# Performance work log

Measured on AMD Instinct MI355X. Metric: run time of the kernel, lower is better.

## Reference

```python
import jax, jax.numpy as jnp
import numpy as np

NEG_SLOPE = 0.1
K = 3  # kernel_size

def lrelu(x):
    return jnp.where(x >= 0, x, NEG_SLOPE * x)

def setup_inputs() -> dict:
    key = jax.random.key(0)
    ks = jax.random.split(key, 10)
    B, C, H, W = 16, 64, 128, 128
    DEG, RED = 512, 8
    s = 0.02
    return {
        "feat": jax.random.normal(ks[0], (B, C, H, W), jnp.float32),
        "deg": jax.random.normal(ks[1], (B, DEG, 8, 8), jnp.float32),
        # adaptive_size: Linear(deg_fsize -> C), no bias; torch weight [out,in]
        "W_size": jax.random.normal(ks[2], (C, DEG), jnp.float32) * s,
        # kernel net: Linear(C -> C//red), Linear(C//red -> C*K*K)
        "W_k1": jax.random.normal(ks[3], (C // RED, C), jnp.float32) * s,
        "W_k2": jax.random.normal(ks[4], (C * K * K, C // RED), jnp.float32) * s,
        # 1x1 conv C_in -> C_out with bias (stored as [out,in])
        "W_conv": jax.random.normal(ks[5], (C, C), jnp.float32) * s,
        "b_conv": jax.random.normal(ks[6], (C,), jnp.float32) * s,
        # CA layer: 1x1 conv deg_fsize -> C, then C -> C//red -> C
        "W_ac": jax.random.normal(ks[7], (C, DEG), jnp.float32) * s,
        "W_du1": jax.random.normal(ks[8], (C // RED, C), jnp.float32) * s,
        "W_du2": jax.random.normal(ks[9], (C, C // RED), jnp.float32) * s,
    }

def reference(feat, deg, W_size, W_k1, W_k2, W_conv, b_conv, W_ac, W_du1, W_du2):
    b, c, h, w = feat.shape
    # degradation pooled to a vector: AdaptiveAvgPool2d((1,1)) == mean over HW
    dvec = deg.mean(axis=(2, 3))                      # [B, deg_fsize]
    f = dvec @ W_size.T                               # [B, C]
    # per-sample dynamic depthwise kernels
    kern = lrelu(f @ W_k1.T) @ W_k2.T                 # [B, C*K*K]
    kern = kern.reshape(b * c, 1, K, K)               # [B*C, 1, K, K]
    out = jax.lax.conv_general_dilated(
        feat.reshape(1, b * c, h, w), kern,
        window_strides=(1, 1), padding=[((K - 1) // 2,) * 2] * 2,
        feature_group_count=b * c,
        dimension_numbers=("NCHW", "OIHW", "NCHW"))
    out = lrelu(out).reshape(b, c, h, w)
    # trailing 1x1 conv with bias
    out = jnp.einsum("bchw,oc->bohw", out, W_conv) + b_conv[None, :, None, None]
    # CA branch
    fa = dvec @ W_ac.T                                # [B, C]
    att = jax.nn.sigmoid(lrelu(fa @ W_du1.T) @ W_du2.T)  # [B, C_out]
    return out + feat * att[:, :, None, None]
```

## Files before the change

### kernel.cpp

```cpp
#include <hip/hip_runtime.h>
#include <math.h>

#define NEG_SLOPE 0.1f

typedef __attribute__((ext_vector_type(8))) short short8;
typedef __attribute__((ext_vector_type(4))) short short4v;
typedef __attribute__((ext_vector_type(4))) float floatx4;

__device__ __forceinline__ float lrelu(float x) { return x >= 0.0f ? x : NEG_SLOPE * x; }

__device__ __forceinline__ unsigned short f2bf(float x) {
  unsigned u = __float_as_uint(x);
  return (unsigned short)((u + 0x7fffu + ((u >> 16) & 1u)) >> 16);
}

__device__ __forceinline__ float wave_sum64(float v) {
  #pragma unroll
  for (int s = 32; s > 0; s >>= 1) v += __shfl_xor(v, s, 64);
  return v;
}

__global__ __launch_bounds__(256) void prep1_kernel(
    const float* __restrict__ deg, float* __restrict__ dvec_ws) {
  const int k = blockIdx.x;
  const int b = k >> 2, quar = k & 3;
  const int t = threadIdx.x;
  const int rw = t >> 1, half = t & 1;
  const int d = quar * 128 + rw;
  const float* p = deg + (size_t)b * 32768 + (size_t)d * 64 + half * 32;
  float4 x0 = *(const float4*)(p);
  float4 x1 = *(const float4*)(p + 4);
  float4 x2 = *(const float4*)(p + 8);
  float4 x3 = *(const float4*)(p + 12);
  float4 x4 = *(const float4*)(p + 16);
  float4 x5 = *(const float4*)(p + 20);
  float4 x6 = *(const float4*)(p + 24);
  float4 x7 = *(const float4*)(p + 28);
  float s = (x0.x + x0.y + x0.z + x0.w) + (x1.x + x1.y + x1.z + x1.w) +
            (x2.x + x2.y + x2.z + x2.w) + (x3.x + x3.y + x3.z + x3.w) +
            (x4.x + x4.y + x4.z + x4.w) + (x5.x + x5.y + x5.z + x5.w) +
            (x6.x + x6.y + x6.z + x6.w) + (x7.x + x7.y + x7.z + x7.w);
  s += __shfl_xor(s, 1, 64);
  if (half == 0) dvec_ws[b * 512 + d] = s * (1.0f / 64.0f);
}

__global__ __launch_bounds__(256) void prep2_kernel(
    const float* __restrict__ dvec_ws, const float* __restrict__ W_size,
    const float* __restrict__ W_ac, float* __restrict__ f_ws,
    float* __restrict__ fa_ws) {
  const int k = blockIdx.x;
  const int b = k >> 2, cq = k & 3;
  const int t = threadIdx.x;
  const int cl = t >> 4, sub = t & 15;
  const int c = cq * 16 + cl;
  const float* dv = dvec_ws + b * 512;
  const float* w1 = W_size + (size_t)c * 512;
  const float* w2 = W_ac + (size_t)c * 512;
  float p1 = 0.0f, p2 = 0.0f;
  #pragma unroll
  for (int kk = 0; kk < 8; ++kk) {
    const int e = sub * 4 + kk * 64;
    float4 d  = *(const float4*)(dv + e);
    float4 a  = *(const float4*)(w1 + e);
    float4 bq = *(const float4*)(w2 + e);
    p1 += d.x * a.x + d.y * a.y + d.z * a.z + d.w * a.w;
    p2 += d.x * bq.x + d.y * bq.y + d.z * bq.z + d.w * bq.w;
  }
  #pragma unroll
  for (int s = 1; s < 16; s <<= 1) {
    p1 += __shfl_xor(p1, s, 64);
    p2 += __shfl_xor(p2, s, 64);
  }
  if (sub == 0) { f_ws[b * 64 + c] = p1; fa_ws[b * 64 + c] = p2; }
}

__global__ __launch_bounds__(256) void prep3_kernel(
    const float* __restrict__ f_ws, const float* __restrict__ fa_ws,
    const float* __restrict__ W_k1, const float* __restrict__ W_k2,
    const float* __restrict__ W_du1, const float* __restrict__ W_du2,
    float* __restrict__ kern_ws, float* __restrict__ att_ws) {
  const int b = blockIdx.x;
  const int t = threadIdx.x;
  __shared__ float t1s[8], t2s[8];
  const int wave = t >> 6, lane = t & 63;
  if (wave == 0) {
    float v = f_ws[b * 64 + lane];
    #pragma unroll
    for (int rr = 0; rr < 8; ++rr) {
      float p = wave_sum64(v * W_k1[rr * 64 + lane]);
      if (lane == 0) t1s[rr] = lrelu(p);
    }
  } else if (wave == 1) {
    float v = fa_ws[b * 64 + lane];
    #pragma unroll
    for (int rr = 0; rr < 8; ++rr) {
      float p = wave_sum64(v * W_du1[rr * 64 + lane]);
      if (lane == 0) t2s[rr] = lrelu(p);
    }
  }
  __syncthreads();
  for (int i = t; i < 576; i += 256) {
    float4 wa0 = *(const float4*)&W_k2[i * 8];
    float4 wa1 = *(const float4*)&W_k2[i * 8 + 4];
    kern_ws[b * 576 + i] =
        t1s[0] * wa0.x + t1s[1] * wa0.y + t1s[2] * wa0.z + t1s[3] * wa0.w +
        t1s[4] * wa1.x + t1s[5] * wa1.y + t1s[6] * wa1.z + t1s[7] * wa1.w;
  }
  if (t < 64) {
    float4 wa0 = *(const float4*)&W_du2[t * 8];
    float4 wa1 = *(const float4*)&W_du2[t * 8 + 4];
    float s = t2s[0] * wa0.x + t2s[1] * wa0.y + t2s[2] * wa0.z + t2s[3] * wa0.w +
              t2s[4] * wa1.x + t2s[5] * wa1.y + t2s[6] * wa1.z + t2s[7] * wa1.w;
    att_ws[b * 64 + t] = 1.0f / (1.0f + expf(-s));
  }
}

__global__ __launch_bounds__(256, 4) void fused_kernel(
    const float* __restrict__ feat, const float* __restrict__ W_conv,
    const float* __restrict__ b_conv, const float* __restrict__ kern_ws,
    const float* __restrict__ att_ws, float* __restrict__ out) {
  const int bid = blockIdx.x;
  const int xcd = bid & 7;
  const int idx = bid >> 3;
  const int b = idx >> 3;
  const int sub = idx & 7;
  const int h_base = xcd * 16 + sub * 2;

  const int t = threadIdx.x;

  __shared__ __align__(16) unsigned short zT[128 * 72];
  __shared__ __align__(16) unsigned short wt[64 * 72];
  __shared__ float ks[576];
  __shared__ float atts[64];
  __shared__ float bcs[64];

  {
    const int o = t >> 2;
    const int c0 = (t & 3) * 16;
    const float* wp = W_conv + o * 64 + c0;
    float4 a0 = *(const float4*)(wp);
    float4 a1 = *(const float4*)(wp + 4);
    float4 a2 = *(const float4*)(wp + 8);
    float4 a3 = *(const float4*)(wp + 12);
    const int sw = ((o >> 2) ^ (o >> 5)) & 7;
    short8 p0, p1;
    p0[0] = f2bf(a0.x); p0[1] = f2bf(a0.y); p0[2] = f2bf(a0.z); p0[3] = f2bf(a0.w);
    p0[4] = f2bf(a1.x); p0[5] = f2bf(a1.y); p0[6] = f2bf(a1.z); p0[7] = f2bf(a1.w);
    p1[0] = f2bf(a2.x); p1[1] = f2bf(a2.y); p1[2] = f2bf(a2.z); p1[3] = f2bf(a2.w);
    p1[4] = f2bf(a3.x); p1[5] = f2bf(a3.y); p1[6] = f2bf(a3.z); p1[7] = f2bf(a3.w);
    const int kc0 = ((c0 >> 3) + 0) ^ sw;
    const int kc1 = ((c0 >> 3) + 1) ^ sw;
    *(short8*)&wt[o * 72 + kc0 * 8] = p0;
    *(short8*)&wt[o * 72 + kc1 * 8] = p1;
  }
  for (int i = t; i < 576; i += 256) ks[i] = kern_ws[b * 576 + i];
  if (t < 64) { atts[t] = att_ws[b * 64 + t]; bcs[t] = b_conv[t]; }
  __syncthreads();

  const size_t base_b = (size_t)b * 64 * 128 * 128;
  const int lane = t & 63, wave = t >> 6;
  const int cq = t >> 5;
  const int gg = t & 31;
  const int w0 = gg * 4;
  const int swz = (gg ^ (gg >> 3)) & 7;
  const float4 zf4 = {0.f, 0.f, 0.f, 0.f};

  #pragma unroll 1
  for (int ti = 0; ti < 2; ++ti) {
    const int h = h_base + ti;
    const bool hgt0 = (h > 0), hlt = (h < 127);
    const float* fbase = feat + base_b + (size_t)h * 128 + w0;

    #pragma unroll
    for (int it = 0; it < 2; ++it) {
      const int c0 = cq * 4 + it * 32;
      float4 top[4], mid[4], bot[4];
      #pragma unroll
      for (int j = 0; j < 4; ++j) {
        const float* p = fbase + (size_t)(c0 + j) * 16384;
        mid[j] = *(const float4*)p;
        top[j] = hgt0 ? *(const float4*)(p - 128) : zf4;
        bot[j] = hlt  ? *(const float4*)(p + 128) : zf4;
      }
      unsigned short sres[4][4];
      #pragma unroll
      for (int j = 0; j < 4; ++j) {
        const float* kv = &ks[(c0 + j) * 9];
        const float k0 = kv[0], k1 = kv[1], k2 = kv[2];
        const float k3 = kv[3], k4 = kv[4], k5 = kv[5];
        const float k6 = kv[6], k7 = kv[7], k8 = kv[8];
        float a0 = 0.f, a1 = 0.f, a2 = 0.f, a3 = 0.f;
        {
          float4 m = top[j];
          float lf = __shfl(m.w, lane - 1, 64); if (gg == 0)  lf = 0.f;
          float rt = __shfl(m.x, lane + 1, 64); if (gg == 31) rt = 0.f;
          a0 += k0 * lf  + k1 * m.x + k2 * m.y;
          a1 += k0 * m.x + k1 * m.y + k2 * m.z;
          a2 += k0 * m.y + k1 * m.z + k2 * m.w;
          a3 += k0 * m.z + k1 * m.w + k2 * rt;
        }
        {
          float4 m = mid[j];
          float lf = __shfl(m.w, lane - 1, 64); if (gg == 0)  lf = 0.f;
          float rt = __shfl(m.x, lane + 1, 64); if (gg == 31) rt = 0.f;
          a0 += k3 * lf  + k4 * m.x + k5 * m.y;
          a1 += k3 * m.x + k4 * m.y + k5 * m.z;
          a2 += k3 * m.y + k4 * m.z + k5 * m.w;
          a3 += k3 * m.z + k4 * m.w + k5 * rt;
        }
        {
          float4 m = bot[j];
          float lf = __shfl(m.w, lane - 1, 64); if (gg == 0)  lf = 0.f;
          float rt = __shfl(m.x, lane + 1, 64); if (gg == 31) rt = 0.f;
          a0 += k6 * lf  + k7 * m.x + k8 * m.y;
          a1 += k6 * m.x + k7 * m.y + k8 * m.z;
          a2 += k6 * m.y + k7 * m.z + k8 * m.w;
          a3 += k6 * m.z + k7 * m.w + k8 * rt;
        }
        sres[j][0] = f2bf(lrelu(a0));
        sres[j][1] = f2bf(lrelu(a1));
        sres[j][2] = f2bf(lrelu(a2));
        sres[j][3] = f2bf(lrelu(a3));
      }
      const int chunk = (cq >> 1) + it * 4;
      const int kcs = ((chunk ^ swz) * 8) + (cq & 1) * 4;
      #pragma unroll
      for (int i = 0; i < 4; ++i) {
        short4v sv;
        sv[0] = (short)sres[0][i]; sv[1] = (short)sres[1][i];
        sv[2] = (short)sres[2][i]; sv[3] = (short)sres[3][i];
        *(short4v*)&zT[(w0 + i) * 72 + kcs] = sv;
      }
    }
    __syncthreads();

    {
      const int r = lane & 15, q = lane >> 4;

      short8 az[2][2];
      #pragma unroll
      for (int wm2 = 0; wm2 < 2; ++wm2) {
        const int w = (wave * 2 + wm2) * 16 + r;
        const int sz = ((w >> 2) ^ (w >> 5)) & 7;
        #pragma unroll
        for (int ksp = 0; ksp < 2; ++ksp) {
          const int kc = (ksp * 4 + q) ^ sz;
          az[wm2][ksp] = *(const short8*)&zT[w * 72 + kc * 8];
        }
      }
      short8 bw[4][2];
      #pragma unroll
      for (int nt = 0; nt < 4; ++nt) {
        const int o = nt * 16 + r;
        const int so = ((o >> 2) ^ (o >> 5)) & 7;
        #pragma unroll
        for (int ksp = 0; ksp < 2; ++ksp) {
          const int kc = (ksp * 4 + q) ^ so;
          bw[nt][ksp] = *(const short8*)&wt[o * 72 + kc * 8];
        }
      }

      floatx4 acc[2][4];
      #pragma unroll
      for (int wm2 = 0; wm2 < 2; ++wm2)
        #pragma unroll
        for (int nt = 0; nt < 4; ++nt) acc[wm2][nt] = (floatx4){0.f, 0.f, 0.f, 0.f};

      #pragma unroll
      for (int wm2 = 0; wm2 < 2; ++wm2)
        #pragma unroll
        for (int nt = 0; nt < 4; ++nt)
          #pragma unroll
          for (int ksp = 0; ksp < 2; ++ksp)
            acc[wm2][nt] = __builtin_amdgcn_mfma_f32_16x16x32_bf16(
                az[wm2][ksp], bw[nt][ksp], acc[wm2][nt], 0, 0, 0);

      #pragma unroll
      for (int wm2 = 0; wm2 < 2; ++wm2) {
        const int wb = (wave * 2 + wm2) * 16 + q * 4;
        #pragma unroll
        for (int nt = 0; nt < 4; ++nt) {
          const int o = nt * 16 + r;
          const size_t off = base_b + (size_t)o * 16384 + (size_t)h * 128 + wb;
          float4 fv = *(const float4*)(feat + off);
          const float at = atts[o], bo = bcs[o];
          floatx4 a = acc[wm2][nt];
          float4 ov;
          ov.x = a[0] + bo + at * fv.x;
          ov.y = a[1] + bo + at * fv.y;
          ov.z = a[2] + bo + at * fv.z;
          ov.w = a[3] + bo + at * fv.w;
          *(float4*)(out + off) = ov;
        }
      }
    }
    if (ti == 0) __syncthreads();
  }
}

extern "C" void kernel_launch(void* const* d_in, const int* in_sizes, int n_in,
                              void* d_out, int out_size, void* d_ws, size_t ws_size,
                              hipStream_t stream) {
  const float* feat   = (const float*)d_in[0];
  const float* deg    = (const float*)d_in[1];
  const float* W_size = (const float*)d_in[2];
  const float* W_k1   = (const float*)d_in[3];
  const float* W_k2   = (const float*)d_in[4];
  const float* W_conv = (const float*)d_in[5];
  const float* b_conv = (const float*)d_in[6];
  const float* W_ac   = (const float*)d_in[7];
  const float* W_du1  = (const float*)d_in[8];
  const float* W_du2  = (const float*)d_in[9];
  float* out = (float*)d_out;

  float* dvec_ws = (float*)d_ws;
  float* f_ws    = dvec_ws + 16 * 512;
  float* fa_ws   = f_ws + 16 * 64;
  float* kern_ws = fa_ws + 16 * 64;
  float* att_ws  = kern_ws + 16 * 576;

  prep1_kernel<<<64, 256, 0, stream>>>(deg, dvec_ws);
  prep2_kernel<<<64, 256, 0, stream>>>(dvec_ws, W_size, W_ac, f_ws, fa_ws);
  prep3_kernel<<<16, 256, 0, stream>>>(f_ws, fa_ws, W_k1, W_k2, W_du1, W_du2,
                                       kern_ws, att_ws);
  fused_kernel<<<1024, 256, 0, stream>>>(feat, W_conv, b_conv, kern_ws, att_ws,
                                         out);
}
```

Measured before the change: 183.0 us.

## Merge prep kernels into one and assign one row per fused block

The three small prep kernels become a single kernel per batch that keeps intermediates in shared memory, removing two launches and their global round trips. The fused kernel now handles one output row per block (2048 blocks) instead of two rows, and the XCD-aware row mapping is replaced with a plain b/h mapping. Launch bounds are raised to 5 blocks per CU. The trade-off is that each block loads and swizzles W_conv and the kernel taps for half as much work, only 16 blocks do the prep stage, and neighbouring rows may no longer share L2 on the same XCD.

```diff
diff --git a/kernel.cpp b/kernel.cpp
--- a/kernel.cpp
+++ b/kernel.cpp
@@ -20,78 +20,71 @@
   return v;
 }
 
-__global__ __launch_bounds__(256) void prep1_kernel(
-    const float* __restrict__ deg, float* __restrict__ dvec_ws) {
-  const int k = blockIdx.x;
-  const int b = k >> 2, quar = k & 3;
-  const int t = threadIdx.x;
-  const int rw = t >> 1, half = t & 1;
-  const int d = quar * 128 + rw;
-  const float* p = deg + (size_t)b * 32768 + (size_t)d * 64 + half * 32;
-  float4 x0 = *(const float4*)(p);
-  float4 x1 = *(const float4*)(p + 4);
-  float4 x2 = *(const float4*)(p + 8);
-  float4 x3 = *(const float4*)(p + 12);
-  float4 x4 = *(const float4*)(p + 16);
-  float4 x5 = *(const float4*)(p + 20);
-  float4 x6 = *(const float4*)(p + 24);
-  float4 x7 = *(const float4*)(p + 28);
-  float s = (x0.x + x0.y + x0.z + x0.w) + (x1.x + x1.y + x1.z + x1.w) +
-            (x2.x + x2.y + x2.z + x2.w) + (x3.x + x3.y + x3.z + x3.w) +
-            (x4.x + x4.y + x4.z + x4.w) + (x5.x + x5.y + x5.z + x5.w) +
-            (x6.x + x6.y + x6.z + x6.w) + (x7.x + x7.y + x7.z + x7.w);
-  s += __shfl_xor(s, 1, 64);
-  if (half == 0) dvec_ws[b * 512 + d] = s * (1.0f / 64.0f);
-}
-
-__global__ __launch_bounds__(256) void prep2_kernel(
-    const float* __restrict__ dvec_ws, const float* __restrict__ W_size,
-    const float* __restrict__ W_ac, float* __restrict__ f_ws,
-    float* __restrict__ fa_ws) {
-  const int k = blockIdx.x;
-  const int b = k >> 2, cq = k & 3;
-  const int t = threadIdx.x;
-  const int cl = t >> 4, sub = t & 15;
-  const int c = cq * 16 + cl;
-  const float* dv = dvec_ws + b * 512;
-  const float* w1 = W_size + (size_t)c * 512;
-  const float* w2 = W_ac + (size_t)c * 512;
-  float p1 = 0.0f, p2 = 0.0f;
-  #pragma unroll
-  for (int kk = 0; kk < 8; ++kk) {
-    const int e = sub * 4 + kk * 64;
-    float4 d  = *(const float4*)(dv + e);
-    float4 a  = *(const float4*)(w1 + e);
-    float4 bq = *(const float4*)(w2 + e);
-    p1 += d.x * a.x + d.y * a.y + d.z * a.z + d.w * a.w;
-    p2 += d.x * bq.x + d.y * bq.y + d.z * bq.z + d.w * bq.w;
-  }
-  #pragma unroll
-  for (int s = 1; s < 16; s <<= 1) {
-    p1 += __shfl_xor(p1, s, 64);
-    p2 += __shfl_xor(p2, s, 64);
-  }
-  if (sub == 0) { f_ws[b * 64 + c] = p1; fa_ws[b * 64 + c] = p2; }
-}
-
-__global__ __launch_bounds__(256) void prep3_kernel(
-    const float* __restrict__ f_ws, const float* __restrict__ fa_ws,
+__global__ __launch_bounds__(256) void prep_kernel(
+    const float* __restrict__ deg, const float* __restrict__ W_size,
     const float* __restrict__ W_k1, const float* __restrict__ W_k2,
-    const float* __restrict__ W_du1, const float* __restrict__ W_du2,
-    float* __restrict__ kern_ws, float* __restrict__ att_ws) {
+    const float* __restrict__ W_ac, const float* __restrict__ W_du1,
+    const float* __restrict__ W_du2, float* __restrict__ kern_ws,
+    float* __restrict__ att_ws) {
   const int b = blockIdx.x;
   const int t = threadIdx.x;
+  __shared__ float dvec[512];
+  __shared__ float fbuf[64], fabuf[64];
   __shared__ float t1s[8], t2s[8];
+
+  const float* degb = deg + (size_t)b * 32768;
+  const int half = t & 1, row0 = t >> 1;
+  #pragma unroll
+  for (int u = 0; u < 4; ++u) {
+    const int d = row0 + u * 128;
+    const float* p = degb + (size_t)d * 64 + half * 32;
+    float4 x0 = *(const float4*)(p);
+    float4 x1 = *(const float4*)(p + 4);
+    float4 x2 = *(const float4*)(p + 8);
+    float4 x3 = *(const float4*)(p + 12);
+    float4 x4 = *(const float4*)(p + 16);
+    float4 x5 = *(const float4*)(p + 20);
+    float4 x6 = *(const float4*)(p + 24);
+    float4 x7 = *(const float4*)(p + 28);
+    float s = (x0.x + x0.y + x0.z + x0.w) + (x1.x + x1.y + x1.z + x1.w) +
+              (x2.x + x2.y + x2.z + x2.w) + (x3.x + x3.y + x3.z + x3.w) +
+              (x4.x + x4.y + x4.z + x4.w) + (x5.x + x5.y + x5.z + x5.w) +
+              (x6.x + x6.y + x6.z + x6.w) + (x7.x + x7.y + x7.z + x7.w);
+    s += __shfl_xor(s, 1, 64);
+    if (half == 0) dvec[d] = s * (1.0f / 64.0f);
+  }
+  __syncthreads();
+
+  {
+    const int c = t >> 2, q = t & 3;
+    const float* w1 = W_size + (size_t)c * 512;
+    const float* w2 = W_ac + (size_t)c * 512;
+    float p1 = 0.0f, p2 = 0.0f;
+    #pragma unroll 4
+    for (int kk = 0; kk < 32; ++kk) {
+      const int e = kk * 16 + q * 4;
+      float4 d4 = *(const float4*)&dvec[e];
+      float4 a4 = *(const float4*)(w1 + e);
+      float4 b4 = *(const float4*)(w2 + e);
+      p1 += d4.x * a4.x + d4.y * a4.y + d4.z * a4.z + d4.w * a4.w;
+      p2 += d4.x * b4.x + d4.y * b4.y + d4.z * b4.z + d4.w * b4.w;
+    }
+    p1 += __shfl_xor(p1, 1, 64); p1 += __shfl_xor(p1, 2, 64);
+    p2 += __shfl_xor(p2, 1, 64); p2 += __shfl_xor(p2, 2, 64);
+    if (q == 0) { fbuf[c] = p1; fabuf[c] = p2; }
+  }
+  __syncthreads();
+
   const int wave = t >> 6, lane = t & 63;
   if (wave == 0) {
-    float v = f_ws[b * 64 + lane];
+    float v = fbuf[lane];
     #pragma unroll
     for (int rr = 0; rr < 8; ++rr) {
       float p = wave_sum64(v * W_k1[rr * 64 + lane]);
       if (lane == 0) t1s[rr] = lrelu(p);
     }
   } else if (wave == 1) {
-    float v = fa_ws[b * 64 + lane];
+    float v = fabuf[lane];
     #pragma unroll
     for (int rr = 0; rr < 8; ++rr) {
       float p = wave_sum64(v * W_du1[rr * 64 + lane]);
@@ -99,6 +92,7 @@
     }
   }
   __syncthreads();
+
   for (int i = t; i < 576; i += 256) {
     float4 wa0 = *(const float4*)&W_k2[i * 8];
     float4 wa1 = *(const float4*)&W_k2[i * 8 + 4];
@@ -115,16 +109,13 @@
   }
 }
 
-__global__ __launch_bounds__(256, 4) void fused_kernel(
+__global__ __launch_bounds__(256, 5) void fused_kernel(
     const float* __restrict__ feat, const float* __restrict__ W_conv,
     const float* __restrict__ b_conv, const float* __restrict__ kern_ws,
     const float* __restrict__ att_ws, float* __restrict__ out) {
   const int bid = blockIdx.x;
-  const int xcd = bid & 7;
-  const int idx = bid >> 3;
-  const int b = idx >> 3;
-  const int sub = idx & 7;
-  const int h_base = xcd * 16 + sub * 2;
+  const int b = bid >> 7;
+  const int h = bid & 127;
 
   const int t = threadIdx.x;
 
@@ -165,136 +156,131 @@
   const int swz = (gg ^ (gg >> 3)) & 7;
   const float4 zf4 = {0.f, 0.f, 0.f, 0.f};
 
-  #pragma unroll 1
-  for (int ti = 0; ti < 2; ++ti) {
-    const int h = h_base + ti;
-    const bool hgt0 = (h > 0), hlt = (h < 127);
-    const float* fbase = feat + base_b + (size_t)h * 128 + w0;
-
-    #pragma unroll
-    for (int it = 0; it < 2; ++it) {
-      const int c0 = cq * 4 + it * 32;
-      float4 top[4], mid[4], bot[4];
-      #pragma unroll
-      for (int j = 0; j < 4; ++j) {
-        const float* p = fbase + (size_t)(c0 + j) * 16384;
-        mid[j] = *(const float4*)p;
-        top[j] = hgt0 ? *(const float4*)(p - 128) : zf4;
-        bot[j] = hlt  ? *(const float4*)(p + 128) : zf4;
-      }
-      unsigned short sres[4][4];
-      #pragma unroll
-      for (int j = 0; j < 4; ++j) {
-        const float* kv = &ks[(c0 + j) * 9];
-        const float k0 = kv[0], k1 = kv[1], k2 = kv[2];
-        const float k3 = kv[3], k4 = kv[4], k5 = kv[5];
-        const float k6 = kv[6], k7 = kv[7], k8 = kv[8];
-        float a0 = 0.f, a1 = 0.f, a2 = 0.f, a3 = 0.f;
-        {
-          float4 m = top[j];
-          float lf = __shfl(m.w, lane - 1, 64); if (gg == 0)  lf = 0.f;
-          float rt = __shfl(m.x, lane + 1, 64); if (gg == 31) rt = 0.f;
-          a0 += k0 * lf  + k1 * m.x + k2 * m.y;
-          a1 += k0 * m.x + k1 * m.y + k2 * m.z;
-          a2 += k0 * m.y + k1 * m.z + k2 * m.w;
-          a3 += k0 * m.z + k1 * m.w + k2 * rt;
-        }
-        {
-          float4 m = mid[j];
-          float lf = __shfl(m.w, lane - 1, 64); if (gg == 0)  lf = 0.f;
-          float rt = __shfl(m.x, lane + 1, 64); if (gg == 31) rt = 0.f;
-          a0 += k3 * lf  + k4 * m.x + k5 * m.y;
-          a1 += k3 * m.x + k4 * m.y + k5 * m.z;
-          a2 += k3 * m.y + k4 * m.z + k5 * m.w;
-          a3 += k3 * m.z + k4 * m.w + k5 * rt;
-        }
-        {
-          float4 m = bot[j];
-          float lf = __shfl(m.w, lane - 1, 64); if (gg == 0)  lf = 0.f;
-          float rt = __shfl(m.x, lane + 1, 64); if (gg == 31) rt = 0.f;
-          a0 += k6 * lf  + k7 * m.x + k8 * m.y;
-          a1 += k6 * m.x + k7 * m.y + k8 * m.z;
-          a2 += k6 * m.y + k7 * m.z + k8 * m.w;
-          a3 += k6 * m.z + k7 * m.w + k8 * rt;
-        }
-        sres[j][0] = f2bf(lrelu(a0));
-        sres[j][1] = f2bf(lrelu(a1));
-        sres[j][2] = f2bf(lrelu(a2));
-        sres[j][3] = f2bf(lrelu(a3));
-      }
-      const int chunk = (cq >> 1) + it * 4;
-      const int kcs = ((chunk ^ swz) * 8) + (cq & 1) * 4;
-      #pragma unroll
-      for (int i = 0; i < 4; ++i) {
-        short4v sv;
-        sv[0] = (short)sres[0][i]; sv[1] = (short)sres[1][i];
-        sv[2] = (short)sres[2][i]; sv[3] = (short)sres[3][i];
-        *(short4v*)&zT[(w0 + i) * 72 + kcs] = sv;
-      }
-    }
-    __syncthreads();
-
-    {
-      const int r = lane & 15, q = lane >> 4;
-
-      short8 az[2][2];
-      #pragma unroll
-      for (int wm2 = 0; wm2 < 2; ++wm2) {
-        const int w = (wave * 2 + wm2) * 16 + r;
-        const int sz = ((w >> 2) ^ (w >> 5)) & 7;
+  const bool hgt0 = (h > 0), hlt = (h < 127);
+  const float* fbase = feat + base_b + (size_t)h * 128 + w0;
+
+  #pragma unroll
+  for (int it = 0; it < 2; ++it) {
+    const int c0 = cq * 4 + it * 32;
+    float4 top[4], mid[4], bot[4];
+    #pragma unroll
+    for (int j = 0; j < 4; ++j) {
+      const float* p = fbase + (size_t)(c0 + j) * 16384;
+      mid[j] = *(const float4*)p;
+      top[j] = hgt0 ? *(const float4*)(p - 128) : zf4;
+      bot[j] = hlt  ? *(const float4*)(p + 128) : zf4;
+    }
+    unsigned short sres[4][4];
+    #pragma unroll
+    for (int j = 0; j < 4; ++j) {
+      const float* kv = &ks[(c0 + j) * 9];
+      const float k0 = kv[0], k1 = kv[1], k2 = kv[2];
+      const float k3 = kv[3], k4 = kv[4], k5 = kv[5];
+      const float k6 = kv[6], k7 = kv[7], k8 = kv[8];
+      float a0 = 0.f, a1 = 0.f, a2 = 0.f, a3 = 0.f;
+      {
+        float4 m = top[j];
+        float lf = __shfl(m.w, lane - 1, 64); if (gg == 0)  lf = 0.f;
+        float rt = __shfl(m.x, lane + 1, 64); if (gg == 31) rt = 0.f;
+        a0 += k0 * lf  + k1 * m.x + k2 * m.y;
+        a1 += k0 * m.x + k1 * m.y + k2 * m.z;
+        a2 += k0 * m.y + k1 * m.z + k2 * m.w;
+        a3 += k0 * m.z + k1 * m.w + k2 * rt;
+      }
+      {
+        float4 m = mid[j];
+        float lf = __shfl(m.w, lane - 1, 64); if (gg == 0)  lf = 0.f;
+        float rt = __shfl(m.x, lane + 1, 64); if (gg == 31) rt = 0.f;
+        a0 += k3 * lf  + k4 * m.x + k5 * m.y;
+        a1 += k3 * m.x + k4 * m.y + k5 * m.z;
+        a2 += k3 * m.y + k4 * m.z + k5 * m.w;
+        a3 += k3 * m.z + k4 * m.w + k5 * rt;
+      }
+      {
+        float4 m = bot[j];
+        float lf = __shfl(m.w, lane - 1, 64); if (gg == 0)  lf = 0.f;
+        float rt = __shfl(m.x, lane + 1, 64); if (gg == 31) rt = 0.f;
+        a0 += k6 * lf  + k7 * m.x + k8 * m.y;
+        a1 += k6 * m.x + k7 * m.y + k8 * m.z;
+        a2 += k6 * m.y + k7 * m.z + k8 * m.w;
+        a3 += k6 * m.z + k7 * m.w + k8 * rt;
+      }
+      sres[j][0] = f2bf(lrelu(a0));
+      sres[j][1] = f2bf(lrelu(a1));
+      sres[j][2] = f2bf(lrelu(a2));
+      sres[j][3] = f2bf(lrelu(a3));
+    }
+    const int chunk = (cq >> 1) + it * 4;
+    const int kcs = ((chunk ^ swz) * 8) + (cq & 1) * 4;
+    #pragma unroll
+    for (int i = 0; i < 4; ++i) {
+      short4v sv;
+      sv[0] = (short)sres[0][i]; sv[1] = (short)sres[1][i];
+      sv[2] = (short)sres[2][i]; sv[3] = (short)sres[3][i];
+      *(short4v*)&zT[(w0 + i) * 72 + kcs] = sv;
+    }
+  }
+  __syncthreads();
+
+  {
+    const int r = lane & 15, q = lane >> 4;
+
+    short8 az[2][2];
+    #pragma unroll
+    for (int wm2 = 0; wm2 < 2; ++wm2) {
+      const int w = (wave * 2 + wm2) * 16 + r;
+      const int sz = ((w >> 2) ^ (w >> 5)) & 7;
+      #pragma unroll
+      for (int ksp = 0; ksp < 2; ++ksp) {
+        const int kc = (ksp * 4 + q) ^ sz;
+        az[wm2][ksp] = *(const short8*)&zT[w * 72 + kc * 8];
+      }
+    }
+    short8 bw[4][2];
+    #pragma unroll
+    for (int nt = 0; nt < 4; ++nt) {
+      const int o = nt * 16 + r;
+      const int so = ((o >> 2) ^ (o >> 5)) & 7;
+      #pragma unroll
+      for (int ksp = 0; ksp < 2; ++ksp) {
+        const int kc = (ksp * 4 + q) ^ so;
+        bw[nt][ksp] = *(const short8*)&wt[o * 72 + kc * 8];
+      }
+    }
+
+    floatx4 acc[2][4];
+    #pragma unroll
+    for (int wm2 = 0; wm2 < 2; ++wm2)
+      #pragma unroll
+      for (int nt = 0; nt < 4; ++nt) acc[wm2][nt] = (floatx4){0.f, 0.f, 0.f, 0.f};
+
+    #pragma unroll
+    for (int wm2 = 0; wm2 < 2; ++wm2)
+      #pragma unroll
+      for (int nt = 0; nt < 4; ++nt)
         #pragma unroll
-        for (int ksp = 0; ksp < 2; ++ksp) {
-          const int kc = (ksp * 4 + q) ^ sz;
-          az[wm2][ksp] = *(const short8*)&zT[w * 72 + kc * 8];
-        }
-      }
-      short8 bw[4][2];
+        for (int ksp = 0; ksp < 2; ++ksp)
+          acc[wm2][nt] = __builtin_amdgcn_mfma_f32_16x16x32_bf16(
+              az[wm2][ksp], bw[nt][ksp], acc[wm2][nt], 0, 0, 0);
+
+    #pragma unroll
+    for (int wm2 = 0; wm2 < 2; ++wm2) {
+      const int wb = (wave * 2 + wm2) * 16 + q * 4;
       #pragma unroll
       for (int nt = 0; nt < 4; ++nt) {
         const int o = nt * 16 + r;
-        const int so = ((o >> 2) ^ (o >> 5)) & 7;
-        #pragma unroll
-        for (int ksp = 0; ksp < 2; ++ksp) {
-          const int kc = (ksp * 4 + q) ^ so;
-          bw[nt][ksp] = *(const short8*)&wt[o * 72 + kc * 8];
-        }
-      }
-
-      floatx4 acc[2][4];
-      #pragma unroll
-      for (int wm2 = 0; wm2 < 2; ++wm2)
-        #pragma unroll
-        for (int nt = 0; nt < 4; ++nt) acc[wm2][nt] = (floatx4){0.f, 0.f, 0.f, 0.f};
-
-      #pragma unroll
-      for (int wm2 = 0; wm2 < 2; ++wm2)
-        #pragma unroll
-        for (int nt = 0; nt < 4; ++nt)
-          #pragma unroll
-          for (int ksp = 0; ksp < 2; ++ksp)
-            acc[wm2][nt] = __builtin_amdgcn_mfma_f32_16x16x32_bf16(
-                az[wm2][ksp], bw[nt][ksp], acc[wm2][nt], 0, 0, 0);
-
-      #pragma unroll
-      for (int wm2 = 0; wm2 < 2; ++wm2) {
-        const int wb = (wave * 2 + wm2) * 16 + q * 4;
-        #pragma unroll
-        for (int nt = 0; nt < 4; ++nt) {
-          const int o = nt * 16 + r;
-          const size_t off = base_b + (size_t)o * 16384 + (size_t)h * 128 + wb;
-          float4 fv = *(const float4*)(feat + off);
-          const float at = atts[o], bo = bcs[o];
-          floatx4 a = acc[wm2][nt];
-          float4 ov;
-          ov.x = a[0] + bo + at * fv.x;
-          ov.y = a[1] + bo + at * fv.y;
-          ov.z = a[2] + bo + at * fv.z;
-          ov.w = a[3] + bo + at * fv.w;
-          *(float4*)(out + off) = ov;
-        }
-      }
-    }
-    if (ti == 0) __syncthreads();
+        const size_t off = base_b + (size_t)o * 16384 + (size_t)h * 128 + wb;
+        float4 fv = *(const float4*)(feat + off);
+        const float at = atts[o], bo = bcs[o];
+        floatx4 a = acc[wm2][nt];
+        float4 ov;
+        ov.x = a[0] + bo + at * fv.x;
+        ov.y = a[1] + bo + at * fv.y;
+        ov.z = a[2] + bo + at * fv.z;
+        ov.w = a[3] + bo + at * fv.w;
+        *(float4*)(out + off) = ov;
+      }
+    }
   }
 }
 
@@ -313,16 +299,11 @@
   const float* W_du2  = (const float*)d_in[9];
   float* out = (float*)d_out;
 
-  float* dvec_ws = (float*)d_ws;
-  float* f_ws    = dvec_ws + 16 * 512;
-  float* fa_ws   = f_ws + 16 * 64;
-  float* kern_ws = fa_ws + 16 * 64;
+  float* kern_ws = (float*)d_ws;
   float* att_ws  = kern_ws + 16 * 576;
 
-  prep1_kernel<<<64, 256, 0, stream>>>(deg, dvec_ws);
-  prep2_kernel<<<64, 256, 0, stream>>>(dvec_ws, W_size, W_ac, f_ws, fa_ws);
-  prep3_kernel<<<16, 256, 0, stream>>>(f_ws, fa_ws, W_k1, W_k2, W_du1, W_du2,
-                                       kern_ws, att_ws);
-  fused_kernel<<<1024, 256, 0, stream>>>(feat, W_conv, b_conv, kern_ws, att_ws,
+  prep_kernel<<<16, 256, 0, stream>>>(deg, W_size, W_k1, W_k2, W_ac, W_du1,
+                                      W_du2, kern_ws, att_ws);
+  fused_kernel<<<2048, 256, 0, stream>>>(feat, W_conv, b_conv, kern_ws, att_ws,
                                          out);
 }
```

Result: no change. 180.7 us (-1.2%).
